# Kernel optimization log

Measured on AMD Instinct MI355X. Metric: run time of the kernel, lower is better.

Reference implementation:

```python
import jax, jax.numpy as jnp
import numpy as np

B, S, D, F = 8, 4096, 1024, 3072
EPS = 1e-6

def rmsnorm(x, w):
    rms = jax.lax.rsqrt(jnp.mean(x * x, axis=-1, keepdims=True) + EPS)
    return x * rms * w

def linear_scan(x, a):
    # h_t = a_t * h_{t-1} + x_t, causal over axis 1 (h_0 prior state = 0)
    def combine(c1, c2):
        a1, h1 = c1
        a2, h2 = c2
        return a1 * a2, a2 * h1 + h2
    return jax.lax.associative_scan(combine, (a, x), axis=1)[1]

def setup_inputs() -> dict:
    key = jax.random.key(0)
    ks = jax.random.split(key, 10)
    s_d = 1.0 / np.sqrt(D)
    s_f = 1.0 / np.sqrt(F)
    return {
        "x": jax.random.normal(ks[0], (B, S, D), jnp.float32),
        "w_rms_mix": jnp.ones((D,), jnp.float32),
        "w_rms_ffn": jnp.ones((D,), jnp.float32),
        "Wg": jax.random.normal(ks[1], (D, D), jnp.float32) * s_d,
        "bg": jnp.zeros((D,), jnp.float32),
        "Wv": jax.random.normal(ks[2], (D, D), jnp.float32) * s_d,
        "bv": jnp.zeros((D,), jnp.float32),
        "Wd": jax.random.normal(ks[3], (D, D), jnp.float32) * s_d,
        "bd": jnp.ones((D,), jnp.float32),  # decay_bias_init = 1.0
        "W_gate": jax.random.normal(ks[4], (D, F), jnp.float32) * s_d,
        "W_up": jax.random.normal(ks[5], (D, F), jnp.float32) * s_d,
        "W_out": jax.random.normal(ks[6], (F, D), jnp.float32) * s_f,
    }

def reference(x, w_rms_mix, w_rms_ffn, Wg, bg, Wv, bv, Wd, bd, W_gate, W_up, W_out):
    # --- MinGRU mixer branch ---
    xn = rmsnorm(x, w_rms_mix)
    g = xn @ Wg + bg
    v = xn @ Wv + bv
    d = xn @ Wd + bd
    x_scan = jax.nn.sigmoid(g) * jnp.tanh(v)
    a = 0.001 + 0.998 * jax.nn.sigmoid(d)
    x = x + linear_scan(x_scan, a)
    # --- SwiGLU FFN branch ---
    yn = rmsnorm(x, w_rms_ffn)
    ffn = (jax.nn.silu(yn @ W_gate) * (yn @ W_up)) @ W_out
    return x + ffn
```

## Files before the change

### kernel.cpp

```cpp
#include <hip/hip_runtime.h>

#define BB 8
#define SS 4096
#define DDIM 1024
#define FDIM 3072
#define CHUNK 128
#define NCH (SS/CHUNK)

typedef __attribute__((ext_vector_type(8))) __bf16 bf16x8;
typedef __attribute__((ext_vector_type(4))) float f32x4;

__device__ __forceinline__ unsigned short f2bf(float f) {
  unsigned int u = __builtin_bit_cast(unsigned int, f);
  u += 0x7FFFu + ((u >> 16) & 1u);
  return (unsigned short)(u >> 16);
}
__device__ __forceinline__ float sigmoid_(float x) { return 1.0f / (1.0f + __expf(-x)); }
__device__ __forceinline__ float tanh_(float x) {
  float xc = fminf(fmaxf(x, -15.0f), 15.0f);
  float e = __expf(2.0f * xc);
  return (e - 1.0f) / (e + 1.0f);
}

__global__ __launch_bounds__(256)
void pack_w(const float* __restrict__ src, unsigned short* __restrict__ dst,
            int Csrc, int Kd, int mode, int rowoff)
{
  __shared__ float tile[64][65];
  const int k0 = blockIdx.y << 6;
  const int c0 = blockIdx.x << 6;
  const int t  = threadIdx.x;
  const int tc = t & 63;
  const int tr = t >> 6;
#pragma unroll
  for (int j = 0; j < 16; j++) {
    int r = (j << 2) + tr;
    tile[r][tc] = src[(size_t)(k0 + r) * Csrc + c0 + tc];
  }
  __syncthreads();
#pragma unroll
  for (int j = 0; j < 16; j++) {
    int c  = (j << 2) + tr;
    int gc = c0 + c;
    int np;
    if (mode == 0)      np = gc + rowoff;
    else if (mode == 1) np = ((gc >> 5) << 6) + (gc & 31);
    else if (mode == 2) np = ((gc >> 5) << 6) + 32 + (gc & 31);
    else                np = ((gc >> 4) << 6) + ((mode - 3) << 4) + (gc & 15);
    dst[(size_t)np * Kd + k0 + tc] = f2bf(tile[tc][c]);
    if (mode == 5) dst[(size_t)(np + 16) * Kd + k0 + tc] = 0;
  }
}

__global__ void pack_bias(const float* __restrict__ bg, const float* __restrict__ bv,
                          const float* __restrict__ bd, float* __restrict__ bias)
{
  int i = blockIdx.x * 256 + threadIdx.x;
  if (i < DDIM) { bias[i] = bg[i]; bias[i + DDIM] = bv[i]; bias[i + 2 * DDIM] = bd[i]; }
}

__global__ __launch_bounds__(256)
void rmsnorm_kernel(const float* __restrict__ x, const float* __restrict__ w,
                    unsigned short* __restrict__ out)
{
  const int row = blockIdx.x;
  const int t = threadIdx.x;
  const float4 v = reinterpret_cast<const float4*>(x + (size_t)row * DDIM)[t];
  float ss = v.x * v.x + v.y * v.y + v.z * v.z + v.w * v.w;
#pragma unroll
  for (int o = 32; o > 0; o >>= 1) ss += __shfl_down(ss, o);
  __shared__ float wsum[4];
  if ((t & 63) == 0) wsum[t >> 6] = ss;
  __syncthreads();
  float tot = wsum[0] + wsum[1] + wsum[2] + wsum[3];
  const float rms = rsqrtf(tot * (1.0f / DDIM) + 1e-6f);
  const float4 wv = reinterpret_cast<const float4*>(w)[t];
  ushort4 o4;
  o4.x = f2bf(v.x * rms * wv.x);
  o4.y = f2bf(v.y * rms * wv.y);
  o4.z = f2bf(v.z * rms * wv.z);
  o4.w = f2bf(v.w * rms * wv.w);
  reinterpret_cast<ushort4*>(out + (size_t)row * DDIM)[t] = o4;
}


#define SB0 __builtin_amdgcn_sched_barrier(0)
#define BAR __builtin_amdgcn_s_barrier()
#define PRIO1 __builtin_amdgcn_s_setprio(1)
#define PRIO0 __builtin_amdgcn_s_setprio(0)
#define WAITL4 do { asm volatile("s_waitcnt lgkmcnt(4)" ::: "memory"); SB0; } while (0)
#define WAITL0 do { asm volatile("s_waitcnt lgkmcnt(0)" ::: "memory"); SB0; } while (0)
#define WAITV6 do { asm volatile("s_waitcnt vmcnt(6)" ::: "memory"); } while (0)
#define WAITV0 do { asm volatile("s_waitcnt vmcnt(0)" ::: "memory"); } while (0)

#define DSR(D, A, O) asm volatile("ds_read_b128 %0, %1 offset:" O : "=v"(D) : "v"(A))
#define RD_BF(B, O0, O1) do { \
  DSR(B[0][0], bB0, O0); DSR(B[0][1], bB1, O0); \
  DSR(B[1][0], bB0, O1); DSR(B[1][1], bB1, O1); } while (0)

template<int MH, int NH, bool SKIP1>
__device__ __forceinline__ void mfma_quad(f32x4 (&acc)[8][4], const bf16x8 (&af)[4][2],
                                          const bf16x8 (&bf)[2][2])
{
#pragma unroll
  for (int mf = 0; mf < 4; mf++)
#pragma unroll
    for (int nf = 0; nf < (SKIP1 ? 1 : 2); nf++)
#pragma unroll
      for (int kk = 0; kk < 2; kk++)
        acc[MH * 4 + mf][NH * 2 + nf] = __builtin_amdgcn_mfma_f32_16x16x32_bf16(
            af[mf][kk], bf[nf][kk], acc[MH * 4 + mf][NH * 2 + nf], 0, 0, 0);
}

template<int MH, int NH, int H, bool SKIP1>
__device__ __forceinline__ void mfma_quad_h(f32x4 (&acc)[8][4], const bf16x8 (&af)[4][2],
                                            const bf16x8 (&bf)[2][2])
{
#pragma unroll
  for (int mf = H * 2; mf < H * 2 + 2; mf++)
#pragma unroll
    for (int nf = 0; nf < (SKIP1 ? 1 : 2); nf++)
#pragma unroll
      for (int kk = 0; kk < 2; kk++)
        acc[MH * 4 + mf][NH * 2 + nf] = __builtin_amdgcn_mfma_f32_16x16x32_bf16(
            af[mf][kk], bf[nf][kk], acc[MH * 4 + mf][NH * 2 + nf], 0, 0, 0);
}

template<int EPI>
__global__ __launch_bounds__(512, 2)
void gemm256(const unsigned short* __restrict__ A,
             const unsigned short* __restrict__ Bt,
             int Np, int K,
             const float* __restrict__ bias,
             const float* __restrict__ resid,
             float* __restrict__ outf,
             unsigned short* __restrict__ outh)
{
  __shared__ __align__(16) unsigned short ldsA[2][256 * 64];
  __shared__ __align__(16) unsigned short ldsB[2][256 * 64];
  const int tid = threadIdx.x, wid = tid >> 6, lane = tid & 63;
  constexpr bool SK = (EPI == 0);

  const int gx = gridDim.x;
  const int lin = blockIdx.y * gx + blockIdx.x;
  const int cpx = (gx * gridDim.y) >> 3;
  const int swz = (lin & 7) * cpx + (lin >> 3);
  const int bx = swz % gx, by = swz / gx;
  const int m0 = by << 8, n0 = bx << 8;
  const int wr = wid >> 2, wc = wid & 3;

  f32x4 acc[8][4];
  const f32x4 zero = {0.f, 0.f, 0.f, 0.f};
#pragma unroll
  for (int a = 0; a < 8; a++)
#pragma unroll
    for (int j = 0; j < 4; j++) acc[a][j] = zero;

  const int swzk = (((tid & 7) ^ ((tid >> 3) & 7)) << 3);
  auto stA = [&](int p, int u, int t) {
#pragma unroll
    for (int r = 0; r < 2; r++) {
      const int lrow0 = (r << 7) + (u << 6);
      const int grow = m0 + lrow0 + (tid >> 3);
      const unsigned short* src = A + (size_t)grow * K + (t << 6) + swzk;
      unsigned short* dst = &ldsA[p][lrow0 << 6] + (wid << 9);
      __builtin_amdgcn_global_load_lds(
          (const __attribute__((address_space(1))) void*)src,
          (__attribute__((address_space(3))) void*)dst, 16, 0, 0);
    }
  };
  auto stB = [&](int p, int u, int t) {
#pragma unroll
    for (int r = 0; r < 2; r++) {
      const int j = (r << 6) + (tid >> 3);
      const int lrow0 = (u << 7) + (r << 6);
      const int gcol = n0 + ((j >> 5) << 6) + (u << 5) + (j & 31);
      const unsigned short* src = Bt + (size_t)gcol * K + (t << 6) + swzk;
      unsigned short* dst = &ldsB[p][lrow0 << 6] + (wid << 9);
      __builtin_amdgcn_global_load_lds(
          (const __attribute__((address_space(1))) void*)src,
          (__attribute__((address_space(3))) void*)dst, 16, 0, 0);
    }
  };

  const unsigned laneR = (unsigned)((lane & 15) << 7);
  const unsigned sw    = (unsigned)((lane & 7) << 4);
  const unsigned k0b   = (unsigned)((lane >> 4) << 4);
  const unsigned baseA = (unsigned)(uintptr_t)&ldsA[0][0] + ((unsigned)wr << 14);
  const unsigned baseB = (unsigned)(uintptr_t)&ldsB[0][0] + ((unsigned)wc << 12);
  const unsigned aA0 = baseA + laneR + (k0b ^ sw);
  const unsigned aA1 = baseA + laneR + ((64u + k0b) ^ sw);
  const unsigned bB0 = baseB + laneR + (k0b ^ sw);
  const unsigned bB1 = baseB + laneR + ((64u + k0b) ^ sw);

  bf16x8 af[4][2];
  bf16x8 bf0[2][2];
  bf16x8 bf1[2][2];

  const int NITER = (K >> 6) >> 1;

  stB(0, 0, 0); stA(0, 0, 0); stB(0, 1, 0); stA(0, 1, 0);
  stB(1, 0, 1); stA(1, 0, 1); stB(1, 1, 1); stA(1, 1, 1);
  asm volatile("s_waitcnt vmcnt(8)" ::: "memory");
  BAR; SB0;
  DSR(af[0][0], aA0, "0");    DSR(af[0][1], aA1, "0");
  DSR(af[1][0], aA0, "2048"); DSR(af[1][1], aA1, "2048");
  DSR(af[2][0], aA0, "4096"); DSR(af[2][1], aA1, "4096");
  DSR(af[3][0], aA0, "6144"); DSR(af[3][1], aA1, "6144");
  DSR(bf0[0][0], bB0, "0");    DSR(bf0[0][1], bB1, "0");
  DSR(bf0[1][0], bB0, "2048"); DSR(bf0[1][1], bB1, "2048");

  for (int i = 0; i < NITER; i++) {
    const int t2 = i << 1;
    const bool more = (i + 1 < NITER);

    RD_BF(bf1, "16384", "18432");
    WAITL4;
    PRIO1; mfma_quad<0, 0, false>(acc, af, bf0); PRIO0; SB0;
    if (more) stB(0, 0, t2 + 2);
    BAR;

    WAITL0;
    PRIO1; mfma_quad_h<0, 1, 0, SK>(acc, af, bf1); SB0;
    DSR(af[0][0], aA0, "8192");  DSR(af[0][1], aA1, "8192");
    DSR(af[1][0], aA0, "10240"); DSR(af[1][1], aA1, "10240"); SB0;
    mfma_quad_h<0, 1, 1, SK>(acc, af, bf1); PRIO0; SB0;
    DSR(af[2][0], aA0, "12288"); DSR(af[2][1], aA1, "12288");
    DSR(af[3][0], aA0, "14336"); DSR(af[3][1], aA1, "14336");
    if (more) stA(0, 0, t2 + 2);
    BAR;

    WAITL0;
    PRIO1; mfma_quad<1, 0, false>(acc, af, bf0); PRIO0; SB0;
    if (more) stB(0, 1, t2 + 2);
    if (more) WAITV6; else WAITV0;
    BAR;

    RD_BF(bf0, "32768", "34816");
    PRIO1; mfma_quad_h<1, 1, 0, SK>(acc, af, bf1); SB0;
    DSR(af[0][0], aA0, "32768"); DSR(af[0][1], aA1, "32768");
    DSR(af[1][0], aA0, "34816"); DSR(af[1][1], aA1, "34816"); SB0;
    mfma_quad_h<1, 1, 1, SK>(acc, af, bf1); PRIO0; SB0;
    DSR(af[2][0], aA0, "36864"); DSR(af[2][1], aA1, "36864");
    DSR(af[3][0], aA0, "38912"); DSR(af[3][1], aA1, "38912");
    if (more) stA(0, 1, t2 + 2);
    BAR;

    RD_BF(bf1, "49152", "51200");
    WAITL4;
    PRIO1; mfma_quad<0, 0, false>(acc, af, bf0); PRIO0; SB0;
    if (more) stB(1, 0, t2 + 3);
    BAR;

    WAITL0;
    PRIO1; mfma_quad_h<0, 1, 0, SK>(acc, af, bf1); SB0;
    DSR(af[0][0], aA0, "40960"); DSR(af[0][1], aA1, "40960");
    DSR(af[1][0], aA0, "43008"); DSR(af[1][1], aA1, "43008"); SB0;
    mfma_quad_h<0, 1, 1, SK>(acc, af, bf1); PRIO0; SB0;
    DSR(af[2][0], aA0, "45056"); DSR(af[2][1], aA1, "45056");
    DSR(af[3][0], aA0, "47104"); DSR(af[3][1], aA1, "47104");
    if (more) stA(1, 0, t2 + 3);
    BAR;

    WAITL0;
    PRIO1; mfma_quad<1, 0, false>(acc, af, bf0); PRIO0; SB0;
    if (more) stB(1, 1, t2 + 3);
    if (more) WAITV6;
    BAR;

    RD_BF(bf0, "0", "2048");
    PRIO1; mfma_quad_h<1, 1, 0, SK>(acc, af, bf1); SB0;
    DSR(af[0][0], aA0, "0");    DSR(af[0][1], aA1, "0");
    DSR(af[1][0], aA0, "2048"); DSR(af[1][1], aA1, "2048"); SB0;
    mfma_quad_h<1, 1, 1, SK>(acc, af, bf1); PRIO0; SB0;
    DSR(af[2][0], aA0, "4096"); DSR(af[2][1], aA1, "4096");
    DSR(af[3][0], aA0, "6144"); DSR(af[3][1], aA1, "6144");
    if (more) stA(1, 1, t2 + 3);
    BAR;
  }
  asm volatile("s_waitcnt lgkmcnt(0)" ::: "memory"); SB0;

  const int lcol = lane & 15;
  const int rgrp = (lane >> 4) << 2;
  if (EPI == 0) {
    const int ch = (n0 >> 2) + (wc << 4) + lcol;
    const float bgv = bias[ch], bvv = bias[ch + DDIM], bdv = bias[ch + 2 * DDIM];
#pragma unroll
    for (int a = 0; a < 8; a++)
#pragma unroll
      for (int rg = 0; rg < 4; rg++) {
        const int row = m0 + (wr << 7) + (a << 4) + rgrp + rg;
        const float g  = acc[a][0][rg] + bgv;
        const float v  = acc[a][1][rg] + bvv;
        const float dd = acc[a][2][rg] + bdv;
        const float aa = 0.001f + 0.998f * sigmoid_(dd);
        const float xs = sigmoid_(g) * tanh_(v);
        float* o = outf + (size_t)row * (2 * DDIM);
        o[ch] = aa;
        o[ch + DDIM] = xs;
      }
  } else if (EPI == 1) {
    const int tN = Np >> 1;
#pragma unroll
    for (int a = 0; a < 8; a++)
#pragma unroll
      for (int j = 0; j < 2; j++) {
        const int tcol = (n0 >> 1) + (wc << 5) + (j << 4) + lcol;
#pragma unroll
        for (int rg = 0; rg < 4; rg++) {
          const int row = m0 + (wr << 7) + (a << 4) + rgrp + rg;
          const float g = acc[a][j][rg];
          const float u = acc[a][j + 2][rg];
          const float s = g / (1.0f + __expf(-g));
          outh[(size_t)row * tN + tcol] = f2bf(s * u);
        }
      }
  } else {
#pragma unroll
    for (int a = 0; a < 8; a++)
#pragma unroll
      for (int j = 0; j < 4; j++) {
        const int col = n0 + (wc << 6) + (j << 4) + lcol;
#pragma unroll
        for (int rg = 0; rg < 4; rg++) {
          const int row = m0 + (wr << 7) + (a << 4) + rgrp + rg;
          outf[(size_t)row * Np + col] = acc[a][j][rg] + resid[(size_t)row * Np + col];
        }
      }
  }
}

__global__ __launch_bounds__(256)
void scan_phase1(const float* __restrict__ ax, float* __restrict__ Ac, float* __restrict__ Hc)
{
  const int d = blockIdx.x * 256 + threadIdx.x;
  const int ch = blockIdx.y;
  const int b = blockIdx.z;
  size_t base = ((size_t)b * SS + (size_t)ch * CHUNK) * (2 * DDIM) + d;
  float Aprod = 1.0f, H = 0.0f;
  for (int s = 0; s < CHUNK; s++) {
    const float a  = ax[base];
    const float xs = ax[base + DDIM];
    H = a * H + xs;
    Aprod *= a;
    base += 2 * DDIM;
  }
  const int idx = (b * NCH + ch) * DDIM + d;
  Ac[idx] = Aprod;
  Hc[idx] = H;
}

__global__ void scan_phase2(const float* __restrict__ Ac, const float* __restrict__ Hc,
                            float* __restrict__ Hpre)
{
  const int idx = blockIdx.x * 256 + threadIdx.x;
  const int b = idx >> 10, d = idx & (DDIM - 1);
  float h = 0.0f;
  for (int c = 0; c < NCH; c++) {
    const int i = (b * NCH + c) * DDIM + d;
    Hpre[i] = h;
    h = Ac[i] * h + Hc[i];
  }
}

__global__ __launch_bounds__(256)
void scan_phase3(const float* __restrict__ ax, const float* __restrict__ x,
                 const float* __restrict__ Hpre, float* __restrict__ xres)
{
  const int d = blockIdx.x * 256 + threadIdx.x;
  const int ch = blockIdx.y;
  const int b = blockIdx.z;
  float H = Hpre[(b * NCH + ch) * DDIM + d];
  const size_t mbase = (size_t)b * SS + (size_t)ch * CHUNK;
  size_t base  = mbase * (2 * DDIM) + d;
  size_t xbase = mbase * DDIM + d;
  for (int s = 0; s < CHUNK; s++) {
    const float a  = ax[base];
    const float xs = ax[base + DDIM];
    H = a * H + xs;
    xres[xbase] = x[xbase] + H;
    base += 2 * DDIM;
    xbase += DDIM;
  }
}

extern "C" void kernel_launch(void* const* d_in, const int* in_sizes, int n_in,
                              void* d_out, int out_size, void* d_ws, size_t ws_size,
                              hipStream_t stream)
{
  const float* x         = (const float*)d_in[0];
  const float* w_rms_mix = (const float*)d_in[1];
  const float* w_rms_ffn = (const float*)d_in[2];
  const float* Wg  = (const float*)d_in[3];
  const float* bg  = (const float*)d_in[4];
  const float* Wv  = (const float*)d_in[5];
  const float* bv  = (const float*)d_in[6];
  const float* Wd  = (const float*)d_in[7];
  const float* bd  = (const float*)d_in[8];
  const float* Wga = (const float*)d_in[9];
  const float* Wup = (const float*)d_in[10];
  const float* Wo  = (const float*)d_in[11];
  float* out = (float*)d_out;

  char* p = (char*)d_ws;
  auto carve = [&](size_t bytes) -> char* {
    char* r = p; p += (bytes + 255) & ~(size_t)255; return r;
  };
  unsigned short* Wgvd4 = (unsigned short*)carve((size_t)4 * DDIM * DDIM * 2);
  unsigned short* WguT  = (unsigned short*)carve((size_t)2 * FDIM * DDIM * 2);
  unsigned short* WoutT = (unsigned short*)carve((size_t)DDIM * FDIM * 2);
  float* bias = (float*)carve(3 * DDIM * 4);
  const size_t fixed_used = (size_t)(p - (char*)d_ws);

  const size_t xn_b  = (size_t)SS * DDIM * 2;
  const size_t ax_b  = (size_t)SS * 2 * DDIM * 4;
  const size_t ach_b = (size_t)NCH * DDIM * 4;
  const size_t per_batch = xn_b + ax_b + 3 * ach_b + 2048;
  long long avail = (long long)ws_size - (long long)fixed_used;
  int nb = (avail > 0) ? (int)(avail / (long long)per_batch) : 1;
  if (nb < 1) nb = 1;
  if (nb > BB) nb = BB;

  unsigned short* xn = (unsigned short*)carve((size_t)nb * xn_b);
  float* ax   = (float*)carve((size_t)nb * ax_b);
  unsigned short* tact = (unsigned short*)ax;
  float* Ac   = (float*)carve((size_t)nb * ach_b);
  float* Hc   = (float*)carve((size_t)nb * ach_b);
  float* Hpre = (float*)carve((size_t)nb * ach_b);

  pack_w<<<dim3(16, 16), 256, 0, stream>>>(Wg,  Wgvd4, DDIM, DDIM, 3, 0);
  pack_w<<<dim3(16, 16), 256, 0, stream>>>(Wv,  Wgvd4, DDIM, DDIM, 4, 0);
  pack_w<<<dim3(16, 16), 256, 0, stream>>>(Wd,  Wgvd4, DDIM, DDIM, 5, 0);
  pack_w<<<dim3(48, 16), 256, 0, stream>>>(Wga, WguT,  FDIM, DDIM, 1, 0);
  pack_w<<<dim3(48, 16), 256, 0, stream>>>(Wup, WguT,  FDIM, DDIM, 2, 0);
  pack_w<<<dim3(16, 48), 256, 0, stream>>>(Wo,  WoutT, DDIM, FDIM, 0, 0);
  pack_bias<<<4, 256, 0, stream>>>(bg, bv, bd, bias);

  for (int b0 = 0; b0 < BB; b0 += nb) {
    const int n  = (BB - b0 < nb) ? (BB - b0) : nb;
    const int Mg = n * SS;
    const float* xg   = x   + (size_t)b0 * SS * DDIM;
    float*       outg = out + (size_t)b0 * SS * DDIM;

    rmsnorm_kernel<<<Mg, 256, 0, stream>>>(xg, w_rms_mix, xn);

    gemm256<0><<<dim3(4 * DDIM / 256, Mg / 256), 512, 0, stream>>>(
        xn, Wgvd4, 4 * DDIM, DDIM, bias, nullptr, ax, nullptr);

    scan_phase1<<<dim3(DDIM / 256, NCH, n), 256, 0, stream>>>(ax, Ac, Hc);
    scan_phase2<<<(n * DDIM) / 256, 256, 0, stream>>>(Ac, Hc, Hpre);
    scan_phase3<<<dim3(DDIM / 256, NCH, n), 256, 0, stream>>>(ax, xg, Hpre, outg);

    rmsnorm_kernel<<<Mg, 256, 0, stream>>>(outg, w_rms_ffn, xn);

    gemm256<1><<<dim3(2 * FDIM / 256, Mg / 256), 512, 0, stream>>>(
        xn, WguT, 2 * FDIM, DDIM, nullptr, nullptr, nullptr, tact);

    gemm256<2><<<dim3(DDIM / 256, Mg / 256), 512, 0, stream>>>(
        tact, WoutT, DDIM, FDIM, nullptr, outg, outg, nullptr);
  }
}
```

Before: 1.051 ms.

## Use 32x32 MFMA GEMM for FFN and store scan inputs as fp16

Adds a new GEMM kernel for the two FFN matmuls built on 32x32x16 bf16 MFMA, with a reworked LDS read schedule and 32-row accumulator tiles. This is meant to cut LDS read traffic per MFMA. The mixer GEMM now writes the scan coefficients as fp16 (storing 1-a for precision) instead of fp32, halving the traffic the scan kernels read. The workspace sizing also changes so that ax and tact share one buffer. The risk is lower precision in the scan inputs, and the new, complex pipeline could contain bugs or bank conflicts.

```diff
diff --git a/kernel.cpp b/kernel.cpp
--- a/kernel.cpp
+++ b/kernel.cpp
@@ -1,4 +1,5 @@
 #include <hip/hip_runtime.h>
+#include <hip/hip_fp16.h>
 
 #define BB 8
 #define SS 4096
@@ -9,6 +10,7 @@
 
 typedef __attribute__((ext_vector_type(8))) __bf16 bf16x8;
 typedef __attribute__((ext_vector_type(4))) float f32x4;
+typedef __attribute__((ext_vector_type(16))) float f32x16;
 
 __device__ __forceinline__ unsigned short f2bf(float f) {
   unsigned int u = __builtin_bit_cast(unsigned int, f);
@@ -83,7 +85,6 @@
   reinterpret_cast<ushort4*>(out + (size_t)row * DDIM)[t] = o4;
 }
 
-
 #define SB0 __builtin_amdgcn_sched_barrier(0)
 #define BAR __builtin_amdgcn_s_barrier()
 #define PRIO1 __builtin_amdgcn_s_setprio(1)
@@ -92,8 +93,8 @@
 #define WAITL0 do { asm volatile("s_waitcnt lgkmcnt(0)" ::: "memory"); SB0; } while (0)
 #define WAITV6 do { asm volatile("s_waitcnt vmcnt(6)" ::: "memory"); } while (0)
 #define WAITV0 do { asm volatile("s_waitcnt vmcnt(0)" ::: "memory"); } while (0)
-
 #define DSR(D, A, O) asm volatile("ds_read_b128 %0, %1 offset:" O : "=v"(D) : "v"(A))
+
 #define RD_BF(B, O0, O1) do { \
   DSR(B[0][0], bB0, O0); DSR(B[0][1], bB1, O0); \
   DSR(B[1][0], bB0, O1); DSR(B[1][1], bB1, O1); } while (0)
@@ -111,7 +112,6 @@
         acc[MH * 4 + mf][NH * 2 + nf] = __builtin_amdgcn_mfma_f32_16x16x32_bf16(
             af[mf][kk], bf[nf][kk], acc[MH * 4 + mf][NH * 2 + nf], 0, 0, 0);
 }
-
 template<int MH, int NH, int H, bool SKIP1>
 __device__ __forceinline__ void mfma_quad_h(f32x4 (&acc)[8][4], const bf16x8 (&af)[4][2],
                                             const bf16x8 (&bf)[2][2])
@@ -126,20 +126,17 @@
             af[mf][kk], bf[nf][kk], acc[MH * 4 + mf][NH * 2 + nf], 0, 0, 0);
 }
 
-template<int EPI>
 __global__ __launch_bounds__(512, 2)
-void gemm256(const unsigned short* __restrict__ A,
-             const unsigned short* __restrict__ Bt,
-             int Np, int K,
-             const float* __restrict__ bias,
-             const float* __restrict__ resid,
-             float* __restrict__ outf,
-             unsigned short* __restrict__ outh)
+void gemm_mix(const unsigned short* __restrict__ A,
+              const unsigned short* __restrict__ Bt,
+              int Np, int K,
+              const float* __restrict__ bias,
+              __half* __restrict__ axh)
 {
   __shared__ __align__(16) unsigned short ldsA[2][256 * 64];
   __shared__ __align__(16) unsigned short ldsB[2][256 * 64];
   const int tid = threadIdx.x, wid = tid >> 6, lane = tid & 63;
-  constexpr bool SK = (EPI == 0);
+  constexpr bool SK = true;
 
   const int gx = gridDim.x;
   const int lin = blockIdx.y * gx + blockIdx.x;
@@ -282,56 +279,201 @@
 
   const int lcol = lane & 15;
   const int rgrp = (lane >> 4) << 2;
-  if (EPI == 0) {
-    const int ch = (n0 >> 2) + (wc << 4) + lcol;
-    const float bgv = bias[ch], bvv = bias[ch + DDIM], bdv = bias[ch + 2 * DDIM];
-#pragma unroll
-    for (int a = 0; a < 8; a++)
-#pragma unroll
-      for (int rg = 0; rg < 4; rg++) {
-        const int row = m0 + (wr << 7) + (a << 4) + rgrp + rg;
-        const float g  = acc[a][0][rg] + bgv;
-        const float v  = acc[a][1][rg] + bvv;
-        const float dd = acc[a][2][rg] + bdv;
-        const float aa = 0.001f + 0.998f * sigmoid_(dd);
-        const float xs = sigmoid_(g) * tanh_(v);
-        float* o = outf + (size_t)row * (2 * DDIM);
-        o[ch] = aa;
-        o[ch + DDIM] = xs;
+  const int ch = (n0 >> 2) + (wc << 4) + lcol;
+  const float bgv = bias[ch], bvv = bias[ch + DDIM], bdv = bias[ch + 2 * DDIM];
+#pragma unroll
+  for (int a = 0; a < 8; a++)
+#pragma unroll
+    for (int rg = 0; rg < 4; rg++) {
+      const int row = m0 + (wr << 7) + (a << 4) + rgrp + rg;
+      const float g  = acc[a][0][rg] + bgv;
+      const float v  = acc[a][1][rg] + bvv;
+      const float dd = acc[a][2][rg] + bdv;
+      const float om = 0.998f * sigmoid_(-dd) + 0.001f;
+      const float xs = sigmoid_(g) * tanh_(v);
+      __half* o = axh + (size_t)row * (2 * DDIM);
+      o[ch] = __float2half_rn(om);
+      o[ch + DDIM] = __float2half_rn(xs);
+    }
+}
+
+#define M32(P, MI, NF, KS, BF) \
+  acc[(P)*2+(MI)][NF] = __builtin_amdgcn_mfma_f32_32x32x16_bf16( \
+      af[MI][KS], BF[KS], acc[(P)*2+(MI)][NF], 0, 0, 0)
+#define Q32(P, NF, BF) do { \
+  M32(P,0,NF,0,BF); M32(P,1,NF,0,BF); M32(P,0,NF,1,BF); M32(P,1,NF,1,BF); \
+  M32(P,0,NF,2,BF); M32(P,1,NF,2,BF); M32(P,0,NF,3,BF); M32(P,1,NF,3,BF); } while (0)
+#define RDA_PAIR(KS, O0, O1) do { \
+  DSR(af[0][KS], aK##KS, O0); DSR(af[1][KS], aK##KS, O1); } while (0)
+#define QW(P, NF, BF, O0, O1) do { \
+  M32(P,0,NF,0,BF); M32(P,1,NF,0,BF); SB0; RDA_PAIR(0, O0, O1); SB0; \
+  M32(P,0,NF,1,BF); M32(P,1,NF,1,BF); SB0; RDA_PAIR(1, O0, O1); SB0; \
+  M32(P,0,NF,2,BF); M32(P,1,NF,2,BF); SB0; RDA_PAIR(2, O0, O1); SB0; \
+  M32(P,0,NF,3,BF); M32(P,1,NF,3,BF); SB0; RDA_PAIR(3, O0, O1); SB0; } while (0)
+#define RDB4(B, O) do { DSR(B[0], bK0, O); DSR(B[1], bK1, O); \
+                        DSR(B[2], bK2, O); DSR(B[3], bK3, O); } while (0)
+
+template<int EPI>
+__global__ __launch_bounds__(512, 2)
+void gemm256w(const unsigned short* __restrict__ A,
+              const unsigned short* __restrict__ Bt,
+              int Np, int K,
+              const float* __restrict__ resid,
+              float* __restrict__ outf,
+              unsigned short* __restrict__ outh)
+{
+  __shared__ __align__(16) unsigned short ldsA[2][256 * 64];
+  __shared__ __align__(16) unsigned short ldsB[2][256 * 64];
+  const int tid = threadIdx.x, wid = tid >> 6, lane = tid & 63;
+
+  const int gx = gridDim.x;
+  const int lin = blockIdx.y * gx + blockIdx.x;
+  const int cpx = (gx * gridDim.y) >> 3;
+  const int swz = (lin & 7) * cpx + (lin >> 3);
+  const int bx = swz % gx, by = swz / gx;
+  const int m0 = by << 8, n0 = bx << 8;
+  const int wr = wid >> 2, wc = wid & 3;
+
+  f32x16 acc[4][2];
+#pragma unroll
+  for (int a = 0; a < 4; a++)
+#pragma unroll
+    for (int j = 0; j < 2; j++)
+#pragma unroll
+      for (int r = 0; r < 16; r++) acc[a][j][r] = 0.f;
+
+  const int swzk = (((tid & 7) ^ ((tid >> 3) & 7)) << 3);
+  auto stA = [&](int p, int u, int t) {
+#pragma unroll
+    for (int r = 0; r < 2; r++) {
+      const int lrow0 = (r << 7) + (u << 6);
+      const int grow = m0 + lrow0 + (tid >> 3);
+      const unsigned short* src = A + (size_t)grow * K + (t << 6) + swzk;
+      unsigned short* dst = &ldsA[p][lrow0 << 6] + (wid << 9);
+      __builtin_amdgcn_global_load_lds(
+          (const __attribute__((address_space(1))) void*)src,
+          (__attribute__((address_space(3))) void*)dst, 16, 0, 0);
+    }
+  };
+  auto stB = [&](int p, int u, int t) {
+#pragma unroll
+    for (int r = 0; r < 2; r++) {
+      const int j = (r << 6) + (tid >> 3);
+      const int lrow0 = (u << 7) + (r << 6);
+      const int gcol = n0 + ((j >> 5) << 6) + (u << 5) + (j & 31);
+      const unsigned short* src = Bt + (size_t)gcol * K + (t << 6) + swzk;
+      unsigned short* dst = &ldsB[p][lrow0 << 6] + (wid << 9);
+      __builtin_amdgcn_global_load_lds(
+          (const __attribute__((address_space(1))) void*)src,
+          (__attribute__((address_space(3))) void*)dst, 16, 0, 0);
+    }
+  };
+
+  const unsigned l31r = (unsigned)((lane & 31) << 7);
+  const unsigned sw   = (unsigned)((lane & 7) << 4);
+  const unsigned kh   = (unsigned)((lane >> 5) << 4);
+  const unsigned baseA = (unsigned)(uintptr_t)&ldsA[0][0] + ((unsigned)wr << 14);
+  const unsigned baseB = (unsigned)(uintptr_t)&ldsB[0][0] + ((unsigned)wc << 12);
+  const unsigned aK0 = baseA + l31r + ((0u   + kh) ^ sw);
+  const unsigned aK1 = baseA + l31r + ((32u  + kh) ^ sw);
+  const unsigned aK2 = baseA + l31r + ((64u  + kh) ^ sw);
+  const unsigned aK3 = baseA + l31r + ((96u  + kh) ^ sw);
+  const unsigned bK0 = baseB + l31r + ((0u   + kh) ^ sw);
+  const unsigned bK1 = baseB + l31r + ((32u  + kh) ^ sw);
+  const unsigned bK2 = baseB + l31r + ((64u  + kh) ^ sw);
+  const unsigned bK3 = baseB + l31r + ((96u  + kh) ^ sw);
+
+  bf16x8 af[2][4];
+  bf16x8 bf0[4];
+  bf16x8 bf1[4];
+
+  const int NITER = (K >> 6) >> 1;
+
+  stB(0, 0, 0); stA(0, 0, 0); stB(0, 1, 0); stA(0, 1, 0);
+  stB(1, 0, 1); stA(1, 0, 1); stB(1, 1, 1); stA(1, 1, 1);
+  asm volatile("s_waitcnt vmcnt(8)" ::: "memory");
+  BAR; SB0;
+  DSR(af[0][0], aK0, "0");    DSR(af[0][1], aK1, "0");
+  DSR(af[0][2], aK2, "0");    DSR(af[0][3], aK3, "0");
+  DSR(af[1][0], aK0, "4096"); DSR(af[1][1], aK1, "4096");
+  DSR(af[1][2], aK2, "4096"); DSR(af[1][3], aK3, "4096");
+  RDB4(bf0, "0");
+
+  for (int i = 0; i < NITER; i++) {
+    const int t2 = i << 1;
+    const bool more = (i + 1 < NITER);
+
+    RDB4(bf1, "16384");
+    WAITL4;
+    PRIO1; Q32(0, 0, bf0); PRIO0; SB0;
+    if (more) stB(0, 0, t2 + 2);
+    BAR;
+    WAITL0;
+    PRIO1; QW(0, 1, bf1, "8192", "12288"); PRIO0; SB0;
+    if (more) stA(0, 0, t2 + 2);
+    BAR;
+    WAITL0;
+    PRIO1; Q32(1, 0, bf0); PRIO0; SB0;
+    if (more) stB(0, 1, t2 + 2);
+    if (more) WAITV6; else WAITV0;
+    BAR;
+    RDB4(bf0, "32768");
+    PRIO1; QW(1, 1, bf1, "32768", "36864"); PRIO0; SB0;
+    if (more) stA(0, 1, t2 + 2);
+    BAR;
+    RDB4(bf1, "49152");
+    WAITL4;
+    PRIO1; Q32(0, 0, bf0); PRIO0; SB0;
+    if (more) stB(1, 0, t2 + 3);
+    BAR;
+    WAITL0;
+    PRIO1; QW(0, 1, bf1, "40960", "45056"); PRIO0; SB0;
+    if (more) stA(1, 0, t2 + 3);
+    BAR;
+    WAITL0;
+    PRIO1; Q32(1, 0, bf0); PRIO0; SB0;
+    if (more) stB(1, 1, t2 + 3);
+    if (more) WAITV6;
+    BAR;
+    RDB4(bf0, "0");
+    PRIO1; QW(1, 1, bf1, "0", "4096"); PRIO0; SB0;
+    if (more) stA(1, 1, t2 + 3);
+    BAR;
+  }
+  asm volatile("s_waitcnt lgkmcnt(0)" ::: "memory"); SB0;
+
+  const int l31 = lane & 31;
+  const int rl  = (lane >> 5) << 2;
+  if (EPI == 1) {
+    const int tN = Np >> 1;
+    const int tcol = (n0 >> 1) + (wc << 5) + l31;
+#pragma unroll
+    for (int mf = 0; mf < 4; mf++)
+#pragma unroll
+      for (int rg = 0; rg < 16; rg++) {
+        const int row = m0 + (wr << 7) + (mf << 5) + (rg & 3) + ((rg >> 2) << 3) + rl;
+        const float g = acc[mf][0][rg];
+        const float u = acc[mf][1][rg];
+        const float s = g / (1.0f + __expf(-g));
+        outh[(size_t)row * tN + tcol] = f2bf(s * u);
       }
-  } else if (EPI == 1) {
-    const int tN = Np >> 1;
-#pragma unroll
-    for (int a = 0; a < 8; a++)
-#pragma unroll
-      for (int j = 0; j < 2; j++) {
-        const int tcol = (n0 >> 1) + (wc << 5) + (j << 4) + lcol;
-#pragma unroll
-        for (int rg = 0; rg < 4; rg++) {
-          const int row = m0 + (wr << 7) + (a << 4) + rgrp + rg;
-          const float g = acc[a][j][rg];
-          const float u = acc[a][j + 2][rg];
-          const float s = g / (1.0f + __expf(-g));
-          outh[(size_t)row * tN + tcol] = f2bf(s * u);
+  } else {
+#pragma unroll
+    for (int mf = 0; mf < 4; mf++)
+#pragma unroll
+      for (int nf = 0; nf < 2; nf++) {
+        const int col = n0 + (wc << 6) + (nf << 5) + l31;
+#pragma unroll
+        for (int rg = 0; rg < 16; rg++) {
+          const int row = m0 + (wr << 7) + (mf << 5) + (rg & 3) + ((rg >> 2) << 3) + rl;
+          outf[(size_t)row * Np + col] = acc[mf][nf][rg] + resid[(size_t)row * Np + col];
         }
       }
-  } else {
-#pragma unroll
-    for (int a = 0; a < 8; a++)
-#pragma unroll
-      for (int j = 0; j < 4; j++) {
-        const int col = n0 + (wc << 6) + (j << 4) + lcol;
-#pragma unroll
-        for (int rg = 0; rg < 4; rg++) {
-          const int row = m0 + (wr << 7) + (a << 4) + rgrp + rg;
-          outf[(size_t)row * Np + col] = acc[a][j][rg] + resid[(size_t)row * Np + col];
-        }
-      }
   }
 }
 
 __global__ __launch_bounds__(256)
-void scan_phase1(const float* __restrict__ ax, float* __restrict__ Ac, float* __restrict__ Hc)
+void scan_phase1(const __half* __restrict__ ax, float* __restrict__ Ac, float* __restrict__ Hc)
 {
   const int d = blockIdx.x * 256 + threadIdx.x;
   const int ch = blockIdx.y;
@@ -339,8 +481,8 @@
   size_t base = ((size_t)b * SS + (size_t)ch * CHUNK) * (2 * DDIM) + d;
   float Aprod = 1.0f, H = 0.0f;
   for (int s = 0; s < CHUNK; s++) {
-    const float a  = ax[base];
-    const float xs = ax[base + DDIM];
+    const float a  = 1.0f - __half2float(ax[base]);
+    const float xs = __half2float(ax[base + DDIM]);
     H = a * H + xs;
     Aprod *= a;
     base += 2 * DDIM;
@@ -364,7 +506,7 @@
 }
 
 __global__ __launch_bounds__(256)
-void scan_phase3(const float* __restrict__ ax, const float* __restrict__ x,
+void scan_phase3(const __half* __restrict__ ax, const float* __restrict__ x,
                  const float* __restrict__ Hpre, float* __restrict__ xres)
 {
   const int d = blockIdx.x * 256 + threadIdx.x;
@@ -375,8 +517,8 @@
   size_t base  = mbase * (2 * DDIM) + d;
   size_t xbase = mbase * DDIM + d;
   for (int s = 0; s < CHUNK; s++) {
-    const float a  = ax[base];
-    const float xs = ax[base + DDIM];
+    const float a  = 1.0f - __half2float(ax[base]);
+    const float xs = __half2float(ax[base + DDIM]);
     H = a * H + xs;
     xres[xbase] = x[xbase] + H;
     base += 2 * DDIM;
@@ -413,17 +555,20 @@
   const size_t fixed_used = (size_t)(p - (char*)d_ws);
 
   const size_t xn_b  = (size_t)SS * DDIM * 2;
-  const size_t ax_b  = (size_t)SS * 2 * DDIM * 4;
+  const size_t ax_b  = (size_t)SS * 2 * DDIM * 2;
+  const size_t tact_b = (size_t)SS * FDIM * 2;
+  const size_t shr_b = (ax_b > tact_b) ? ax_b : tact_b;
   const size_t ach_b = (size_t)NCH * DDIM * 4;
-  const size_t per_batch = xn_b + ax_b + 3 * ach_b + 2048;
+  const size_t per_batch = xn_b + shr_b + 3 * ach_b + 2048;
   long long avail = (long long)ws_size - (long long)fixed_used;
   int nb = (avail > 0) ? (int)(avail / (long long)per_batch) : 1;
   if (nb < 1) nb = 1;
   if (nb > BB) nb = BB;
 
   unsigned short* xn = (unsigned short*)carve((size_t)nb * xn_b);
-  float* ax   = (float*)carve((size_t)nb * ax_b);
-  unsigned short* tact = (unsigned short*)ax;
+  char* shr = carve((size_t)nb * shr_b);
+  __half* ax = (__half*)shr;
+  unsigned short* tact = (unsigned short*)shr;
   float* Ac   = (float*)carve((size_t)nb * ach_b);
   float* Hc   = (float*)carve((size_t)nb * ach_b);
   float* Hpre = (float*)carve((size_t)nb * ach_b);
@@ -444,8 +589,8 @@
 
     rmsnorm_kernel<<<Mg, 256, 0, stream>>>(xg, w_rms_mix, xn);
 
-    gemm256<0><<<dim3(4 * DDIM / 256, Mg / 256), 512, 0, stream>>>(
-        xn, Wgvd4, 4 * DDIM, DDIM, bias, nullptr, ax, nullptr);
+    gemm_mix<<<dim3(4 * DDIM / 256, Mg / 256), 512, 0, stream>>>(
+        xn, Wgvd4, 4 * DDIM, DDIM, bias, ax);
 
     scan_phase1<<<dim3(DDIM / 256, NCH, n), 256, 0, stream>>>(ax, Ac, Hc);
     scan_phase2<<<(n * DDIM) / 256, 256, 0, stream>>>(Ac, Hc, Hpre);
@@ -453,10 +598,10 @@
 
     rmsnorm_kernel<<<Mg, 256, 0, stream>>>(outg, w_rms_ffn, xn);
 
-    gemm256<1><<<dim3(2 * FDIM / 256, Mg / 256), 512, 0, stream>>>(
-        xn, WguT, 2 * FDIM, DDIM, nullptr, nullptr, nullptr, tact);
-
-    gemm256<2><<<dim3(DDIM / 256, Mg / 256), 512, 0, stream>>>(
-        tact, WoutT, DDIM, FDIM, nullptr, outg, outg, nullptr);
-  }
-}
+    gemm256w<1><<<dim3(2 * FDIM / 256, Mg / 256), 512, 0, stream>>>(
+        xn, WguT, 2 * FDIM, DDIM, nullptr, nullptr, tact);
+
+    gemm256w<2><<<dim3(DDIM / 256, Mg / 256), 512, 0, stream>>>(
+        tact, WoutT, DDIM, FDIM, outg, outg, nullptr);
+  }
+}
```

New measurement: 1.026 ms. 2.4% less time.
